# Kernel tuning notes

Hardware: AMD Instinct MI355X
Metric: run time of the kernel (lower is better)

The kernel has to match this reference:

```python
import jax, jax.numpy as jnp
import numpy as np

Q = 0.25          # magnetic charge q
MAX_EIGEN = 2.0   # max_eigen default

N_NODES = 1024
N_EDGES = 32768
IN_DIM = 128


def setup_inputs() -> dict:
    key = jax.random.key(0)
    k1, k2, k3, k4 = jax.random.split(key, 4)
    features = jax.random.normal(k1, (N_NODES, IN_DIM), dtype=jnp.float32)
    edges = jax.random.randint(k2, (2, N_EDGES), 0, N_NODES, dtype=jnp.int64)
    w_e1 = jax.random.normal(k3, (1, IN_DIM), dtype=jnp.float32) * (1.0 / np.sqrt(IN_DIM))
    b_e1 = jax.random.normal(k4, (1,), dtype=jnp.float32) * 0.01
    return {"features": features, "edges": edges, "w_e1": w_e1, "b_e1": b_e1, "K": 4}


def reference(features, edges, w_e1, b_e1, K):
    N = features.shape[0]
    # e1: Linear(input_dim, 1), then squeeze -> per-node scalar potential p
    p = (features @ w_e1.T + b_e1)[:, 0]                       # [N]
    u, v = edges[0], edges[1]
    val = jnp.maximum(p[u] - p[v], 0.0)                        # [M]
    w = 1.0 + val
    directed = val > 0
    # val == 0 -> self loops (u,u),(v,v); val > 0 -> (u,v),(v,u); weight 1+val each
    rows = jnp.concatenate([u, v])
    cols = jnp.concatenate([jnp.where(directed, v, u), jnp.where(directed, u, v)])
    ww = jnp.concatenate([w, w])
    A = jnp.zeros((N, N), dtype=features.dtype).at[rows, cols].add(ww)
    A = A + jnp.eye(N, dtype=features.dtype)                   # unit-weight self loops (diag_eye)

    A_sym = 0.5 * (A + A.T)
    # symmetric degree normalization (norm=True)
    d = A_sym.sum(axis=0)
    d = jnp.where(d == 0, 1.0, d) ** -0.5
    A_sym = d[:, None] * A_sym * d[None, :]

    # magnetic phase: Theta = exp(2*pi*q*i*(A - A^T))
    Theta = jnp.exp((2j * jnp.pi * Q) * (A - A.T).astype(jnp.complex64))
    I = jnp.eye(N, dtype=jnp.complex64)
    L = I - Theta * A_sym.astype(jnp.complex64)                # D=I since norm=True
    L = (2.0 / MAX_EIGEN) * L - I                              # spectral rescale

    # Chebyshev recursion: T0 = I, T1 = L, T_k = 2 L T_{k-1} - T_{k-2}
    polys = [I, L]
    for _ in range(2, K + 1):
        polys.append(2.0 * (L @ polys[-1]) - polys[-2])
    L_real = jnp.stack([t.real for t in polys])                # [K+1, N, N]
    L_img = jnp.stack([t.imag for t in polys])                 # [K+1, N, N]
    return (L_real, L_img)
```

## Files before the change

kernel.cpp:

```cpp
#include <hip/hip_runtime.h>

#define NPTS 1024
#define NN (NPTS * NPTS)
#define NEDGE 32768
#define INDIM 128
#define PAD 72

typedef __attribute__((ext_vector_type(8))) short bf16x8;
typedef __attribute__((ext_vector_type(4))) float f32x4;

__device__ inline ushort f2bf(float x) {
    union { float f; unsigned u; } v; v.f = x;
    unsigned r = (v.u + 0x7FFF + ((v.u >> 16) & 1)) >> 16;
    return (ushort)r;
}

#define MFMA(a, b, c) __builtin_amdgcn_mfma_f32_16x16x32_bf16(a, b, c, 0, 0, 0)


__global__ void zeroA_p_kernel(float4* __restrict__ A4,
                               const float* __restrict__ feat,
                               const float* __restrict__ w,
                               const float* __restrict__ b,
                               float* __restrict__ p,
                               float4* __restrict__ dd4) {
    int t = threadIdx.x;
    A4[blockIdx.x * 256 + t] = make_float4(0.f, 0.f, 0.f, 0.f);
    if (blockIdx.x == 1024 - 1 && t < 256) dd4[t] = make_float4(0.f, 0.f, 0.f, 0.f);
    if (blockIdx.x < 256) {
        int wid = t >> 6, lane = t & 63;
        int node = blockIdx.x * 4 + wid;
        const float* f = feat + node * INDIM;
        float s = f[lane] * w[lane] + f[lane + 64] * w[lane + 64];
#pragma unroll
        for (int off = 32; off; off >>= 1) s += __shfl_down(s, off);
        if (lane == 0) p[node] = s + b[0];
    }
}

__global__ void build_A_kernel(const int* __restrict__ eu, const int* __restrict__ ev,
                               const float* __restrict__ p, float* __restrict__ A,
                               float* __restrict__ dd) {
    int i = blockIdx.x * blockDim.x + threadIdx.x;
    if (i >= NEDGE) return;
    int u = eu[i], v = ev[i];
    float val = p[u] - p[v];
    if (val > 0.f) {
        float w = 1.f + val;
        atomicAdd(&A[u * NPTS + v], w);
        atomicAdd(&A[v * NPTS + u], w);
        atomicAdd(&dd[u], w);
        atomicAdd(&dd[v], w);
    } else {
        atomicAdd(&A[u * NPTS + u], 1.f);
        atomicAdd(&A[v * NPTS + v], 1.f);
        atomicAdd(&dd[u], 1.f);
        atomicAdd(&dd[v], 1.f);
    }
}

__global__ void normalize_kernel(const float* __restrict__ A, const float* __restrict__ dd,
                                 float* __restrict__ out, ushort* __restrict__ Mbf) {
    int idx4 = blockIdx.x * blockDim.x + threadIdx.x;
    int i = idx4 >> 8;
    int j = (idx4 & 255) * 4;
    size_t idx = (size_t)idx4 * 4;
    float di = rsqrtf(dd[i] + 1.f);
    float4 a = *(const float4*)(A + idx);
    float4 d4 = *(const float4*)(dd + j);
    float4 t0 = make_float4(0.f, 0.f, 0.f, 0.f);
    if (i == j) t0.x = 1.f;
    else if (i == j + 1) t0.y = 1.f;
    else if (i == j + 2) t0.z = 1.f;
    else if (i == j + 3) t0.w = 1.f;
    a.x += (i == j);
    a.y += (i == j + 1);
    a.z += (i == j + 2);
    a.w += (i == j + 3);
    float4 m;
    m.x = -(di * a.x * rsqrtf(d4.x + 1.f));
    m.y = -(di * a.y * rsqrtf(d4.y + 1.f));
    m.z = -(di * a.z * rsqrtf(d4.z + 1.f));
    m.w = -(di * a.w * rsqrtf(d4.w + 1.f));
    *(float4*)(out + idx) = t0;
    *(float4*)(out + NN + idx) = m;
    ushort mb[4] = {f2bf(m.x), f2bf(m.y), f2bf(m.z), f2bf(m.w)};
    *(uint2*)(Mbf + idx) = *(uint2*)mb;
}


__global__ __launch_bounds__(512) void gemm_S_kernel(const ushort* __restrict__ Mbf,
                                                     ushort* __restrict__ Sbf,
                                                     float* __restrict__ out) {
    __shared__ __align__(16) ushort sA[2][64][PAD];
    __shared__ __align__(16) ushort sB[2][64][PAD];

    int tid = threadIdx.x;
    int brow = blockIdx.y * 64, bcol = blockIdx.x * 64;
    int r = tid >> 3, j0 = (tid & 7) * 8;
    int wid = tid >> 6, lane = tid & 63;
    int wr = (wid & 3) * 16, wc = (wid >> 2) * 32;
    int fr = lane & 15, g = lane >> 4;

    const ushort* Arow = Mbf + (size_t)(brow + r) * NPTS;
    const ushort* Brow = Mbf + (size_t)(bcol + r) * NPTS;

    f32x4 acc[2] = {};
    float4 pa = *(const float4*)(Arow + j0);
    float4 pb = *(const float4*)(Brow + j0);
    *(float4*)&sA[0][r][j0] = pa;
    *(float4*)&sB[0][r][j0] = pb;
    pa = *(const float4*)(Arow + 64 + j0);
    pb = *(const float4*)(Brow + 64 + j0);

    const int NT = NPTS / 64;
    for (int t = 0; t < NT; ++t) {
        __syncthreads();
        if (t + 1 < NT) {
            *(float4*)&sA[(t + 1) & 1][r][j0] = pa;
            *(float4*)&sB[(t + 1) & 1][r][j0] = pb;
        }
        if (t + 2 < NT) {
            pa = *(const float4*)(Arow + (t + 2) * 64 + j0);
            pb = *(const float4*)(Brow + (t + 2) * 64 + j0);
        }
        int cb = t & 1;
#pragma unroll
        for (int kc = 0; kc < 2; ++kc) {
            int kk = kc * 32 + g * 8;
            bf16x8 a0 = *(const bf16x8*)&sA[cb][wr + fr][kk];
            bf16x8 b0 = *(const bf16x8*)&sB[cb][wc + fr][kk];
            bf16x8 b1 = *(const bf16x8*)&sB[cb][wc + 16 + fr][kk];
            acc[0] = MFMA(a0, b0, acc[0]);
            acc[1] = MFMA(a0, b1, acc[1]);
        }
    }

    float* T2 = out + (size_t)2 * NN;
#pragma unroll
    for (int ni = 0; ni < 2; ++ni) {
#pragma unroll
        for (int q = 0; q < 4; ++q) {
            int row = brow + wr + g * 4 + q;
            int col = bcol + wc + ni * 16 + fr;
            size_t idx = (size_t)row * NPTS + col;
            float s = acc[ni][q];
            T2[idx] = 2.f * s - (row == col ? 1.f : 0.f);
            Sbf[idx] = f2bf(s);
        }
    }
}

__global__ __launch_bounds__(512) void gemm_T34_kernel(const ushort* __restrict__ Mbf,
                                                       const ushort* __restrict__ Sbf,
                                                       float* __restrict__ out,
                                                       int zimag) {
    if (zimag) {
        int bid = blockIdx.y * 16 + blockIdx.x;
        float4* z = (float4*)(out + (size_t)5 * NN) + (size_t)bid * 5120 + threadIdx.x;
#pragma unroll
        for (int i = 0; i < 10; ++i) z[i * 512] = make_float4(0.f, 0.f, 0.f, 0.f);
    }

    __shared__ __align__(16) ushort sAS[2][64][PAD];
    __shared__ __align__(16) ushort sAM[2][64][PAD];
    __shared__ __align__(16) ushort sB[2][64][PAD];

    int tid = threadIdx.x;
    int brow = blockIdx.y * 64, bcol = blockIdx.x * 64;
    int r = tid >> 3, j0 = (tid & 7) * 8;
    int wid = tid >> 6, lane = tid & 63;
    int wr = (wid & 3) * 16, wc = (wid >> 2) * 32;
    int fr = lane & 15, g = lane >> 4;

    const ushort* ASrow = Sbf + (size_t)(brow + r) * NPTS;
    const ushort* AMrow = Mbf + (size_t)(brow + r) * NPTS;
    const ushort* Brow = Sbf + (size_t)(bcol + r) * NPTS;

    f32x4 accP[2] = {};
    f32x4 accR[2] = {};
    float4 ps = *(const float4*)(ASrow + j0);
    float4 pm = *(const float4*)(AMrow + j0);
    float4 pb = *(const float4*)(Brow + j0);
    *(float4*)&sAS[0][r][j0] = ps;
    *(float4*)&sAM[0][r][j0] = pm;
    *(float4*)&sB[0][r][j0] = pb;
    ps = *(const float4*)(ASrow + 64 + j0);
    pm = *(const float4*)(AMrow + 64 + j0);
    pb = *(const float4*)(Brow + 64 + j0);

    const int NT = NPTS / 64;
    for (int t = 0; t < NT; ++t) {
        __syncthreads();
        if (t + 1 < NT) {
            *(float4*)&sAS[(t + 1) & 1][r][j0] = ps;
            *(float4*)&sAM[(t + 1) & 1][r][j0] = pm;
            *(float4*)&sB[(t + 1) & 1][r][j0] = pb;
        }
        if (t + 2 < NT) {
            int k0 = (t + 2) * 64;
            ps = *(const float4*)(ASrow + k0 + j0);
            pm = *(const float4*)(AMrow + k0 + j0);
            pb = *(const float4*)(Brow + k0 + j0);
        }
        int cb = t & 1;
#pragma unroll
        for (int kc = 0; kc < 2; ++kc) {
            int kk = kc * 32 + g * 8;
            bf16x8 b0 = *(const bf16x8*)&sB[cb][wc + fr][kk];
            bf16x8 b1 = *(const bf16x8*)&sB[cb][wc + 16 + fr][kk];
            bf16x8 s0 = *(const bf16x8*)&sAS[cb][wr + fr][kk];
            bf16x8 m0 = *(const bf16x8*)&sAM[cb][wr + fr][kk];
            accP[0] = MFMA(s0, b0, accP[0]);
            accP[1] = MFMA(s0, b1, accP[1]);
            accR[0] = MFMA(m0, b0, accR[0]);
            accR[1] = MFMA(m0, b1, accR[1]);
        }
    }

    float* T1 = out + (size_t)NN;
    float* T2 = out + (size_t)2 * NN;
    float* T3 = out + (size_t)3 * NN;
    float* T4 = out + (size_t)4 * NN;
#pragma unroll
    for (int ni = 0; ni < 2; ++ni) {
#pragma unroll
        for (int q = 0; q < 4; ++q) {
            int row = brow + wr + g * 4 + q;
            int col = bcol + wc + ni * 16 + fr;
            size_t idx = (size_t)row * NPTS + col;
            float sp = accP[ni][q];
            float sr = accR[ni][q];
            T4[idx] = 8.f * sp - 4.f * T2[idx] - (row == col ? 3.f : 0.f);
            T3[idx] = 4.f * sr - 3.f * T1[idx];
        }
    }
}

__global__ void zero_kernel(float4* __restrict__ p, int n4) {
    int i = blockIdx.x * blockDim.x + threadIdx.x;
    if (i < n4) p[i] = make_float4(0.f, 0.f, 0.f, 0.f);
}


extern "C" void kernel_launch(void* const* d_in, const int* in_sizes, int n_in,
                              void* d_out, int out_size, void* d_ws, size_t ws_size,
                              hipStream_t stream) {
    const float* feat = (const float*)d_in[0];
    const int* edges = (const int*)d_in[1];
    const float* w_e1 = (const float*)d_in[2];
    const float* b_e1 = (const float*)d_in[3];
    float* out = (float*)d_out;

    const size_t need = (size_t)NN * 4 + (size_t)NN * 2 + (size_t)NN * 2 + NPTS * 8 + 256;
    float* A;
    ushort* Mbf;
    ushort* Sbf;
    float* p;
    float* dd;
    int use_ws = (ws_size >= need);
    if (use_ws) {
        char* w = (char*)d_ws;
        A = (float*)w;        w += (size_t)NN * 4;
        Mbf = (ushort*)w;     w += (size_t)NN * 2;
        Sbf = (ushort*)w;     w += (size_t)NN * 2;
        p = (float*)w;        w += NPTS * 4;
        dd = (float*)w;
    } else {
        A = out + (size_t)5 * NN;
        Mbf = (ushort*)(out + (size_t)6 * NN);
        Sbf = Mbf + NN;
        p = out + (size_t)7 * NN;
        dd = p + NPTS;
    }

    zeroA_p_kernel<<<1024, 256, 0, stream>>>((float4*)A, feat, w_e1, b_e1, p, (float4*)dd);
    build_A_kernel<<<(NEDGE + 255) / 256, 256, 0, stream>>>(edges, edges + NEDGE, p, A, dd);
    normalize_kernel<<<NN / 4 / 256, 256, 0, stream>>>(A, dd, out, Mbf);

    dim3 grid(16, 16);
    gemm_S_kernel<<<grid, 512, 0, stream>>>(Mbf, Sbf, out);
    gemm_T34_kernel<<<grid, 512, 0, stream>>>(Mbf, Sbf, out, use_ws);

    if (!use_ws) {
        zero_kernel<<<(5 * NN / 4 + 255) / 256, 256, 0, stream>>>(
            (float4*)(out + (size_t)5 * NN), 5 * NN / 4);
    }
}
```

Before: 59.11 us.

## Use 256-thread GEMM blocks with 2x2 MFMA tiles per wave and single-buffered LDS

Both GEMM kernels now run 4 waves of 256 threads instead of 8 waves of 512, and each wave computes a 32x32 output tile (2x2 MFMA fragments) instead of 16x32. Each A fragment is reused across two B fragments, which cuts LDS reads per MFMA. The LDS double buffer becomes a single buffer with two barriers per k-step, and global prefetch runs only one tile ahead. This lowers shared memory per block and register-level redundancy, but gives up some load/compute overlap and halves the waves per block on a grid of only 256 blocks.

```diff
diff --git a/kernel.cpp b/kernel.cpp
--- a/kernel.cpp
+++ b/kernel.cpp
@@ -26,7 +26,7 @@
                                float4* __restrict__ dd4) {
     int t = threadIdx.x;
     A4[blockIdx.x * 256 + t] = make_float4(0.f, 0.f, 0.f, 0.f);
-    if (blockIdx.x == 1024 - 1 && t < 256) dd4[t] = make_float4(0.f, 0.f, 0.f, 0.f);
+    if (blockIdx.x == 1023 && t < 256) dd4[t] = make_float4(0.f, 0.f, 0.f, 0.f);
     if (blockIdx.x < 256) {
         int wid = t >> 6, lane = t & 63;
         int node = blockIdx.x * 4 + wid;
@@ -89,132 +89,146 @@
 }
 
 
-__global__ __launch_bounds__(512) void gemm_S_kernel(const ushort* __restrict__ Mbf,
-                                                     ushort* __restrict__ Sbf,
-                                                     float* __restrict__ out) {
-    __shared__ __align__(16) ushort sA[2][64][PAD];
-    __shared__ __align__(16) ushort sB[2][64][PAD];
+__global__ __launch_bounds__(256, 2) void gemm_S_kernel(const ushort* __restrict__ Mbf,
+                                                        ushort* __restrict__ Sbf,
+                                                        float* __restrict__ out) {
+    __shared__ __align__(16) ushort sA[64][PAD];
+    __shared__ __align__(16) ushort sB[64][PAD];
 
     int tid = threadIdx.x;
     int brow = blockIdx.y * 64, bcol = blockIdx.x * 64;
-    int r = tid >> 3, j0 = (tid & 7) * 8;
+    int r = tid >> 2, j0 = (tid & 3) * 8;
     int wid = tid >> 6, lane = tid & 63;
-    int wr = (wid & 3) * 16, wc = (wid >> 2) * 32;
+    int wr = (wid & 1) * 32, wc = (wid >> 1) * 32;
     int fr = lane & 15, g = lane >> 4;
 
     const ushort* Arow = Mbf + (size_t)(brow + r) * NPTS;
     const ushort* Brow = Mbf + (size_t)(bcol + r) * NPTS;
 
-    f32x4 acc[2] = {};
-    float4 pa = *(const float4*)(Arow + j0);
-    float4 pb = *(const float4*)(Brow + j0);
-    *(float4*)&sA[0][r][j0] = pa;
-    *(float4*)&sB[0][r][j0] = pb;
-    pa = *(const float4*)(Arow + 64 + j0);
-    pb = *(const float4*)(Brow + 64 + j0);
+    f32x4 acc[2][2] = {};
+    float4 pa0 = *(const float4*)(Arow + j0);
+    float4 pa1 = *(const float4*)(Arow + 32 + j0);
+    float4 pb0 = *(const float4*)(Brow + j0);
+    float4 pb1 = *(const float4*)(Brow + 32 + j0);
 
     const int NT = NPTS / 64;
     for (int t = 0; t < NT; ++t) {
         __syncthreads();
+        *(float4*)&sA[r][j0] = pa0;
+        *(float4*)&sA[r][32 + j0] = pa1;
+        *(float4*)&sB[r][j0] = pb0;
+        *(float4*)&sB[r][32 + j0] = pb1;
+        __syncthreads();
         if (t + 1 < NT) {
-            *(float4*)&sA[(t + 1) & 1][r][j0] = pa;
-            *(float4*)&sB[(t + 1) & 1][r][j0] = pb;
-        }
-        if (t + 2 < NT) {
-            pa = *(const float4*)(Arow + (t + 2) * 64 + j0);
-            pb = *(const float4*)(Brow + (t + 2) * 64 + j0);
-        }
-        int cb = t & 1;
+            int k0 = (t + 1) * 64;
+            pa0 = *(const float4*)(Arow + k0 + j0);
+            pa1 = *(const float4*)(Arow + k0 + 32 + j0);
+            pb0 = *(const float4*)(Brow + k0 + j0);
+            pb1 = *(const float4*)(Brow + k0 + 32 + j0);
+        }
 #pragma unroll
         for (int kc = 0; kc < 2; ++kc) {
             int kk = kc * 32 + g * 8;
-            bf16x8 a0 = *(const bf16x8*)&sA[cb][wr + fr][kk];
-            bf16x8 b0 = *(const bf16x8*)&sB[cb][wc + fr][kk];
-            bf16x8 b1 = *(const bf16x8*)&sB[cb][wc + 16 + fr][kk];
-            acc[0] = MFMA(a0, b0, acc[0]);
-            acc[1] = MFMA(a0, b1, acc[1]);
+            bf16x8 a0 = *(const bf16x8*)&sA[wr + fr][kk];
+            bf16x8 a1 = *(const bf16x8*)&sA[wr + 16 + fr][kk];
+            bf16x8 b0 = *(const bf16x8*)&sB[wc + fr][kk];
+            bf16x8 b1 = *(const bf16x8*)&sB[wc + 16 + fr][kk];
+            acc[0][0] = MFMA(a0, b0, acc[0][0]);
+            acc[0][1] = MFMA(a0, b1, acc[0][1]);
+            acc[1][0] = MFMA(a1, b0, acc[1][0]);
+            acc[1][1] = MFMA(a1, b1, acc[1][1]);
         }
     }
 
     float* T2 = out + (size_t)2 * NN;
 #pragma unroll
-    for (int ni = 0; ni < 2; ++ni) {
-#pragma unroll
-        for (int q = 0; q < 4; ++q) {
-            int row = brow + wr + g * 4 + q;
-            int col = bcol + wc + ni * 16 + fr;
-            size_t idx = (size_t)row * NPTS + col;
-            float s = acc[ni][q];
-            T2[idx] = 2.f * s - (row == col ? 1.f : 0.f);
-            Sbf[idx] = f2bf(s);
-        }
-    }
-}
-
-__global__ __launch_bounds__(512) void gemm_T34_kernel(const ushort* __restrict__ Mbf,
-                                                       const ushort* __restrict__ Sbf,
-                                                       float* __restrict__ out,
-                                                       int zimag) {
+    for (int mi = 0; mi < 2; ++mi) {
+#pragma unroll
+        for (int ni = 0; ni < 2; ++ni) {
+#pragma unroll
+            for (int q = 0; q < 4; ++q) {
+                int row = brow + wr + mi * 16 + g * 4 + q;
+                int col = bcol + wc + ni * 16 + fr;
+                size_t idx = (size_t)row * NPTS + col;
+                float s = acc[mi][ni][q];
+                T2[idx] = 2.f * s - (row == col ? 1.f : 0.f);
+                Sbf[idx] = f2bf(s);
+            }
+        }
+    }
+}
+
+__global__ __launch_bounds__(256, 2) void gemm_T34_kernel(const ushort* __restrict__ Mbf,
+                                                          const ushort* __restrict__ Sbf,
+                                                          float* __restrict__ out,
+                                                          int zimag) {
     if (zimag) {
         int bid = blockIdx.y * 16 + blockIdx.x;
         float4* z = (float4*)(out + (size_t)5 * NN) + (size_t)bid * 5120 + threadIdx.x;
 #pragma unroll
-        for (int i = 0; i < 10; ++i) z[i * 512] = make_float4(0.f, 0.f, 0.f, 0.f);
-    }
-
-    __shared__ __align__(16) ushort sAS[2][64][PAD];
-    __shared__ __align__(16) ushort sAM[2][64][PAD];
-    __shared__ __align__(16) ushort sB[2][64][PAD];
+        for (int i = 0; i < 20; ++i) z[i * 256] = make_float4(0.f, 0.f, 0.f, 0.f);
+    }
+
+    __shared__ __align__(16) ushort sAS[64][PAD];
+    __shared__ __align__(16) ushort sAM[64][PAD];
+    __shared__ __align__(16) ushort sB[64][PAD];
 
     int tid = threadIdx.x;
     int brow = blockIdx.y * 64, bcol = blockIdx.x * 64;
-    int r = tid >> 3, j0 = (tid & 7) * 8;
+    int r = tid >> 2, j0 = (tid & 3) * 8;
     int wid = tid >> 6, lane = tid & 63;
-    int wr = (wid & 3) * 16, wc = (wid >> 2) * 32;
+    int wr = (wid & 1) * 32, wc = (wid >> 1) * 32;
     int fr = lane & 15, g = lane >> 4;
 
     const ushort* ASrow = Sbf + (size_t)(brow + r) * NPTS;
     const ushort* AMrow = Mbf + (size_t)(brow + r) * NPTS;
     const ushort* Brow = Sbf + (size_t)(bcol + r) * NPTS;
 
-    f32x4 accP[2] = {};
-    f32x4 accR[2] = {};
-    float4 ps = *(const float4*)(ASrow + j0);
-    float4 pm = *(const float4*)(AMrow + j0);
-    float4 pb = *(const float4*)(Brow + j0);
-    *(float4*)&sAS[0][r][j0] = ps;
-    *(float4*)&sAM[0][r][j0] = pm;
-    *(float4*)&sB[0][r][j0] = pb;
-    ps = *(const float4*)(ASrow + 64 + j0);
-    pm = *(const float4*)(AMrow + 64 + j0);
-    pb = *(const float4*)(Brow + 64 + j0);
+    f32x4 accP[2][2] = {};
+    f32x4 accR[2][2] = {};
+    float4 ps0 = *(const float4*)(ASrow + j0);
+    float4 ps1 = *(const float4*)(ASrow + 32 + j0);
+    float4 pm0 = *(const float4*)(AMrow + j0);
+    float4 pm1 = *(const float4*)(AMrow + 32 + j0);
+    float4 pb0 = *(const float4*)(Brow + j0);
+    float4 pb1 = *(const float4*)(Brow + 32 + j0);
 
     const int NT = NPTS / 64;
     for (int t = 0; t < NT; ++t) {
         __syncthreads();
+        *(float4*)&sAS[r][j0] = ps0;
+        *(float4*)&sAS[r][32 + j0] = ps1;
+        *(float4*)&sAM[r][j0] = pm0;
+        *(float4*)&sAM[r][32 + j0] = pm1;
+        *(float4*)&sB[r][j0] = pb0;
+        *(float4*)&sB[r][32 + j0] = pb1;
+        __syncthreads();
         if (t + 1 < NT) {
-            *(float4*)&sAS[(t + 1) & 1][r][j0] = ps;
-            *(float4*)&sAM[(t + 1) & 1][r][j0] = pm;
-            *(float4*)&sB[(t + 1) & 1][r][j0] = pb;
-        }
-        if (t + 2 < NT) {
-            int k0 = (t + 2) * 64;
-            ps = *(const float4*)(ASrow + k0 + j0);
-            pm = *(const float4*)(AMrow + k0 + j0);
-            pb = *(const float4*)(Brow + k0 + j0);
-        }
-        int cb = t & 1;
+            int k0 = (t + 1) * 64;
+            ps0 = *(const float4*)(ASrow + k0 + j0);
+            ps1 = *(const float4*)(ASrow + k0 + 32 + j0);
+            pm0 = *(const float4*)(AMrow + k0 + j0);
+            pm1 = *(const float4*)(AMrow + k0 + 32 + j0);
+            pb0 = *(const float4*)(Brow + k0 + j0);
+            pb1 = *(const float4*)(Brow + k0 + 32 + j0);
+        }
 #pragma unroll
         for (int kc = 0; kc < 2; ++kc) {
             int kk = kc * 32 + g * 8;
-            bf16x8 b0 = *(const bf16x8*)&sB[cb][wc + fr][kk];
-            bf16x8 b1 = *(const bf16x8*)&sB[cb][wc + 16 + fr][kk];
-            bf16x8 s0 = *(const bf16x8*)&sAS[cb][wr + fr][kk];
-            bf16x8 m0 = *(const bf16x8*)&sAM[cb][wr + fr][kk];
-            accP[0] = MFMA(s0, b0, accP[0]);
-            accP[1] = MFMA(s0, b1, accP[1]);
-            accR[0] = MFMA(m0, b0, accR[0]);
-            accR[1] = MFMA(m0, b1, accR[1]);
+            bf16x8 b0 = *(const bf16x8*)&sB[wc + fr][kk];
+            bf16x8 b1 = *(const bf16x8*)&sB[wc + 16 + fr][kk];
+            bf16x8 s0 = *(const bf16x8*)&sAS[wr + fr][kk];
+            bf16x8 s1 = *(const bf16x8*)&sAS[wr + 16 + fr][kk];
+            accP[0][0] = MFMA(s0, b0, accP[0][0]);
+            accP[0][1] = MFMA(s0, b1, accP[0][1]);
+            accP[1][0] = MFMA(s1, b0, accP[1][0]);
+            accP[1][1] = MFMA(s1, b1, accP[1][1]);
+            bf16x8 m0 = *(const bf16x8*)&sAM[wr + fr][kk];
+            bf16x8 m1 = *(const bf16x8*)&sAM[wr + 16 + fr][kk];
+            accR[0][0] = MFMA(m0, b0, accR[0][0]);
+            accR[0][1] = MFMA(m0, b1, accR[0][1]);
+            accR[1][0] = MFMA(m1, b0, accR[1][0]);
+            accR[1][1] = MFMA(m1, b1, accR[1][1]);
         }
     }
 
@@ -223,16 +237,19 @@
     float* T3 = out + (size_t)3 * NN;
     float* T4 = out + (size_t)4 * NN;
 #pragma unroll
-    for (int ni = 0; ni < 2; ++ni) {
-#pragma unroll
-        for (int q = 0; q < 4; ++q) {
-            int row = brow + wr + g * 4 + q;
-            int col = bcol + wc + ni * 16 + fr;
-            size_t idx = (size_t)row * NPTS + col;
-            float sp = accP[ni][q];
-            float sr = accR[ni][q];
-            T4[idx] = 8.f * sp - 4.f * T2[idx] - (row == col ? 3.f : 0.f);
-            T3[idx] = 4.f * sr - 3.f * T1[idx];
+    for (int mi = 0; mi < 2; ++mi) {
+#pragma unroll
+        for (int ni = 0; ni < 2; ++ni) {
+#pragma unroll
+            for (int q = 0; q < 4; ++q) {
+                int row = brow + wr + mi * 16 + g * 4 + q;
+                int col = bcol + wc + ni * 16 + fr;
+                size_t idx = (size_t)row * NPTS + col;
+                float sp = accP[mi][ni][q];
+                float sr = accR[mi][ni][q];
+                T4[idx] = 8.f * sp - 4.f * T2[idx] - (row == col ? 3.f : 0.f);
+                T3[idx] = 4.f * sr - 3.f * T1[idx];
+            }
         }
     }
 }
@@ -279,8 +296,8 @@
     normalize_kernel<<<NN / 4 / 256, 256, 0, stream>>>(A, dd, out, Mbf);
 
     dim3 grid(16, 16);
-    gemm_S_kernel<<<grid, 512, 0, stream>>>(Mbf, Sbf, out);
-    gemm_T34_kernel<<<grid, 512, 0, stream>>>(Mbf, Sbf, out, use_ws);
+    gemm_S_kernel<<<grid, 256, 0, stream>>>(Mbf, Sbf, out);
+    gemm_T34_kernel<<<grid, 256, 0, stream>>>(Mbf, Sbf, out, use_ws);
 
     if (!use_ws) {
         zero_kernel<<<(5 * NN / 4 + 255) / 256, 256, 0, stream>>>(
```

New measurement: 69.37 us. 1.17x slower.

## Retile Chebyshev GEMMs to 32x64 blocks with K=128 single-buffered LDS

Applied to the files above, without the earlier changes.

Both bf16 MFMA GEMM kernels move from 64x64 tiles with 512 threads and a double-buffered K=64 LDS pipeline to 32x64 tiles with 256 threads and a single-buffered K=128 stage. The grid doubles to 512 blocks, and the imaginary-zeroing stride is adjusted to match. The aim is more blocks for better CU occupancy and fewer loop iterations. In exchange, each stage now needs two barriers and the register prefetch no longer overlaps with LDS double buffering, and the B tile is reloaded more often because A reuse per block is lower.

```diff
diff --git a/kernel.cpp b/kernel.cpp
--- a/kernel.cpp
+++ b/kernel.cpp
@@ -4,7 +4,7 @@
 #define NN (NPTS * NPTS)
 #define NEDGE 32768
 #define INDIM 128
-#define PAD 72
+#define BKP 136
 
 typedef __attribute__((ext_vector_type(8))) short bf16x8;
 typedef __attribute__((ext_vector_type(4))) float f32x4;
@@ -26,7 +26,7 @@
                                float4* __restrict__ dd4) {
     int t = threadIdx.x;
     A4[blockIdx.x * 256 + t] = make_float4(0.f, 0.f, 0.f, 0.f);
-    if (blockIdx.x == 1024 - 1 && t < 256) dd4[t] = make_float4(0.f, 0.f, 0.f, 0.f);
+    if (blockIdx.x == 1023 && t < 256) dd4[t] = make_float4(0.f, 0.f, 0.f, 0.f);
     if (blockIdx.x < 256) {
         int wid = t >> 6, lane = t & 63;
         int node = blockIdx.x * 4 + wid;
@@ -89,48 +89,57 @@
 }
 
 
-__global__ __launch_bounds__(512) void gemm_S_kernel(const ushort* __restrict__ Mbf,
-                                                     ushort* __restrict__ Sbf,
-                                                     float* __restrict__ out) {
-    __shared__ __align__(16) ushort sA[2][64][PAD];
-    __shared__ __align__(16) ushort sB[2][64][PAD];
+__global__ void gemm_S_kernel(const ushort* __restrict__ Mbf,
+                              ushort* __restrict__ Sbf,
+                              float* __restrict__ out) {
+    __shared__ __align__(16) ushort smem[(32 + 64) * BKP];
+    ushort(*sA)[BKP] = (ushort(*)[BKP])smem;
+    ushort(*sB)[BKP] = (ushort(*)[BKP])(smem + 32 * BKP);
 
     int tid = threadIdx.x;
-    int brow = blockIdx.y * 64, bcol = blockIdx.x * 64;
-    int r = tid >> 3, j0 = (tid & 7) * 8;
+    int brow = blockIdx.y * 32, bcol = blockIdx.x * 64;
+    int ra = tid >> 3, ca = (tid & 7) * 16;
+    int rb = tid >> 2, cb = (tid & 3) * 32;
     int wid = tid >> 6, lane = tid & 63;
-    int wr = (wid & 3) * 16, wc = (wid >> 2) * 32;
+    int wr = (wid & 1) * 16, wc = (wid >> 1) * 32;
     int fr = lane & 15, g = lane >> 4;
 
-    const ushort* Arow = Mbf + (size_t)(brow + r) * NPTS;
-    const ushort* Brow = Mbf + (size_t)(bcol + r) * NPTS;
+    const ushort* Arow = Mbf + (size_t)(brow + ra) * NPTS + ca;
+    const ushort* Brow = Mbf + (size_t)(bcol + rb) * NPTS + cb;
 
     f32x4 acc[2] = {};
-    float4 pa = *(const float4*)(Arow + j0);
-    float4 pb = *(const float4*)(Brow + j0);
-    *(float4*)&sA[0][r][j0] = pa;
-    *(float4*)&sB[0][r][j0] = pb;
-    pa = *(const float4*)(Arow + 64 + j0);
-    pb = *(const float4*)(Brow + 64 + j0);
-
-    const int NT = NPTS / 64;
+    float4 pa0 = *(const float4*)(Arow);
+    float4 pa1 = *(const float4*)(Arow + 8);
+    float4 pb0 = *(const float4*)(Brow);
+    float4 pb1 = *(const float4*)(Brow + 8);
+    float4 pb2 = *(const float4*)(Brow + 16);
+    float4 pb3 = *(const float4*)(Brow + 24);
+
+    const int NT = NPTS / 128;
     for (int t = 0; t < NT; ++t) {
         __syncthreads();
+        *(float4*)&sA[ra][ca] = pa0;
+        *(float4*)&sA[ra][ca + 8] = pa1;
+        *(float4*)&sB[rb][cb] = pb0;
+        *(float4*)&sB[rb][cb + 8] = pb1;
+        *(float4*)&sB[rb][cb + 16] = pb2;
+        *(float4*)&sB[rb][cb + 24] = pb3;
+        __syncthreads();
         if (t + 1 < NT) {
-            *(float4*)&sA[(t + 1) & 1][r][j0] = pa;
-            *(float4*)&sB[(t + 1) & 1][r][j0] = pb;
-        }
-        if (t + 2 < NT) {
-            pa = *(const float4*)(Arow + (t + 2) * 64 + j0);
-            pb = *(const float4*)(Brow + (t + 2) * 64 + j0);
-        }
-        int cb = t & 1;
-#pragma unroll
-        for (int kc = 0; kc < 2; ++kc) {
+            int k0 = (t + 1) * 128;
+            pa0 = *(const float4*)(Arow + k0);
+            pa1 = *(const float4*)(Arow + k0 + 8);
+            pb0 = *(const float4*)(Brow + k0);
+            pb1 = *(const float4*)(Brow + k0 + 8);
+            pb2 = *(const float4*)(Brow + k0 + 16);
+            pb3 = *(const float4*)(Brow + k0 + 24);
+        }
+#pragma unroll
+        for (int kc = 0; kc < 4; ++kc) {
             int kk = kc * 32 + g * 8;
-            bf16x8 a0 = *(const bf16x8*)&sA[cb][wr + fr][kk];
-            bf16x8 b0 = *(const bf16x8*)&sB[cb][wc + fr][kk];
-            bf16x8 b1 = *(const bf16x8*)&sB[cb][wc + 16 + fr][kk];
+            bf16x8 a0 = *(const bf16x8*)&sA[wr + fr][kk];
+            bf16x8 b0 = *(const bf16x8*)&sB[wc + fr][kk];
+            bf16x8 b1 = *(const bf16x8*)&sB[wc + 16 + fr][kk];
             acc[0] = MFMA(a0, b0, acc[0]);
             acc[1] = MFMA(a0, b1, acc[1]);
         }
@@ -151,66 +160,75 @@
     }
 }
 
-__global__ __launch_bounds__(512) void gemm_T34_kernel(const ushort* __restrict__ Mbf,
-                                                       const ushort* __restrict__ Sbf,
-                                                       float* __restrict__ out,
-                                                       int zimag) {
+__global__ void gemm_T34_kernel(const ushort* __restrict__ Mbf,
+                                const ushort* __restrict__ Sbf,
+                                float* __restrict__ out,
+                                int zimag) {
     if (zimag) {
         int bid = blockIdx.y * 16 + blockIdx.x;
-        float4* z = (float4*)(out + (size_t)5 * NN) + (size_t)bid * 5120 + threadIdx.x;
-#pragma unroll
-        for (int i = 0; i < 10; ++i) z[i * 512] = make_float4(0.f, 0.f, 0.f, 0.f);
-    }
-
-    __shared__ __align__(16) ushort sAS[2][64][PAD];
-    __shared__ __align__(16) ushort sAM[2][64][PAD];
-    __shared__ __align__(16) ushort sB[2][64][PAD];
+        float4* z = (float4*)(out + (size_t)5 * NN) + (size_t)bid * 2560 + threadIdx.x;
+#pragma unroll
+        for (int i = 0; i < 10; ++i) z[i * 256] = make_float4(0.f, 0.f, 0.f, 0.f);
+    }
+
+    __shared__ __align__(16) ushort smem[(32 + 32 + 64) * BKP];
+    ushort(*sAS)[BKP] = (ushort(*)[BKP])smem;
+    ushort(*sAM)[BKP] = (ushort(*)[BKP])(smem + 32 * BKP);
+    ushort(*sB)[BKP] = (ushort(*)[BKP])(smem + 64 * BKP);
 
     int tid = threadIdx.x;
-    int brow = blockIdx.y * 64, bcol = blockIdx.x * 64;
-    int r = tid >> 3, j0 = (tid & 7) * 8;
+    int brow = blockIdx.y * 32, bcol = blockIdx.x * 64;
+    int ra = tid >> 3, ca = (tid & 7) * 16;
+    int rb = tid >> 2, cb = (tid & 3) * 32;
     int wid = tid >> 6, lane = tid & 63;
-    int wr = (wid & 3) * 16, wc = (wid >> 2) * 32;
+    int wr = (wid & 1) * 16, wc = (wid >> 1) * 32;
     int fr = lane & 15, g = lane >> 4;
 
-    const ushort* ASrow = Sbf + (size_t)(brow + r) * NPTS;
-    const ushort* AMrow = Mbf + (size_t)(brow + r) * NPTS;
-    const ushort* Brow = Sbf + (size_t)(bcol + r) * NPTS;
+    const ushort* ASrow = Sbf + (size_t)(brow + ra) * NPTS + ca;
+    const ushort* AMrow = Mbf + (size_t)(brow + ra) * NPTS + ca;
+    const ushort* Brow = Sbf + (size_t)(bcol + rb) * NPTS + cb;
 
     f32x4 accP[2] = {};
     f32x4 accR[2] = {};
-    float4 ps = *(const float4*)(ASrow + j0);
-    float4 pm = *(const float4*)(AMrow + j0);
-    float4 pb = *(const float4*)(Brow + j0);
-    *(float4*)&sAS[0][r][j0] = ps;
-    *(float4*)&sAM[0][r][j0] = pm;
-    *(float4*)&sB[0][r][j0] = pb;
-    ps = *(const float4*)(ASrow + 64 + j0);
-    pm = *(const float4*)(AMrow + 64 + j0);
-    pb = *(const float4*)(Brow + 64 + j0);
-
-    const int NT = NPTS / 64;
+    float4 ps0 = *(const float4*)(ASrow);
+    float4 ps1 = *(const float4*)(ASrow + 8);
+    float4 pm0 = *(const float4*)(AMrow);
+    float4 pm1 = *(const float4*)(AMrow + 8);
+    float4 pb0 = *(const float4*)(Brow);
+    float4 pb1 = *(const float4*)(Brow + 8);
+    float4 pb2 = *(const float4*)(Brow + 16);
+    float4 pb3 = *(const float4*)(Brow + 24);
+
+    const int NT = NPTS / 128;
     for (int t = 0; t < NT; ++t) {
         __syncthreads();
+        *(float4*)&sAS[ra][ca] = ps0;
+        *(float4*)&sAS[ra][ca + 8] = ps1;
+        *(float4*)&sAM[ra][ca] = pm0;
+        *(float4*)&sAM[ra][ca + 8] = pm1;
+        *(float4*)&sB[rb][cb] = pb0;
+        *(float4*)&sB[rb][cb + 8] = pb1;
+        *(float4*)&sB[rb][cb + 16] = pb2;
+        *(float4*)&sB[rb][cb + 24] = pb3;
+        __syncthreads();
         if (t + 1 < NT) {
-            *(float4*)&sAS[(t + 1) & 1][r][j0] = ps;
-            *(float4*)&sAM[(t + 1) & 1][r][j0] = pm;
-            *(float4*)&sB[(t + 1) & 1][r][j0] = pb;
-        }
-        if (t + 2 < NT) {
-            int k0 = (t + 2) * 64;
-            ps = *(const float4*)(ASrow + k0 + j0);
-            pm = *(const float4*)(AMrow + k0 + j0);
-            pb = *(const float4*)(Brow + k0 + j0);
-        }
-        int cb = t & 1;
-#pragma unroll
-        for (int kc = 0; kc < 2; ++kc) {
+            int k0 = (t + 1) * 128;
+            ps0 = *(const float4*)(ASrow + k0);
+            ps1 = *(const float4*)(ASrow + k0 + 8);
+            pm0 = *(const float4*)(AMrow + k0);
+            pm1 = *(const float4*)(AMrow + k0 + 8);
+            pb0 = *(const float4*)(Brow + k0);
+            pb1 = *(const float4*)(Brow + k0 + 8);
+            pb2 = *(const float4*)(Brow + k0 + 16);
+            pb3 = *(const float4*)(Brow + k0 + 24);
+        }
+#pragma unroll
+        for (int kc = 0; kc < 4; ++kc) {
             int kk = kc * 32 + g * 8;
-            bf16x8 b0 = *(const bf16x8*)&sB[cb][wc + fr][kk];
-            bf16x8 b1 = *(const bf16x8*)&sB[cb][wc + 16 + fr][kk];
-            bf16x8 s0 = *(const bf16x8*)&sAS[cb][wr + fr][kk];
-            bf16x8 m0 = *(const bf16x8*)&sAM[cb][wr + fr][kk];
+            bf16x8 b0 = *(const bf16x8*)&sB[wc + fr][kk];
+            bf16x8 b1 = *(const bf16x8*)&sB[wc + 16 + fr][kk];
+            bf16x8 s0 = *(const bf16x8*)&sAS[wr + fr][kk];
+            bf16x8 m0 = *(const bf16x8*)&sAM[wr + fr][kk];
             accP[0] = MFMA(s0, b0, accP[0]);
             accP[1] = MFMA(s0, b1, accP[1]);
             accR[0] = MFMA(m0, b0, accR[0]);
@@ -278,9 +296,9 @@
     build_A_kernel<<<(NEDGE + 255) / 256, 256, 0, stream>>>(edges, edges + NEDGE, p, A, dd);
     normalize_kernel<<<NN / 4 / 256, 256, 0, stream>>>(A, dd, out, Mbf);
 
-    dim3 grid(16, 16);
-    gemm_S_kernel<<<grid, 512, 0, stream>>>(Mbf, Sbf, out);
-    gemm_T34_kernel<<<grid, 512, 0, stream>>>(Mbf, Sbf, out, use_ws);
+    dim3 grid(16, 32);
+    gemm_S_kernel<<<grid, 256, 0, stream>>>(Mbf, Sbf, out);
+    gemm_T34_kernel<<<grid, 256, 0, stream>>>(Mbf, Sbf, out, use_ws);
 
     if (!use_ws) {
         zero_kernel<<<(5 * NN / 4 + 255) / 256, 256, 0, stream>>>(
```

New measurement: 61.89 us. 1.05x slower.
